# Optimization experiments

Measured on AMD Instinct MI355X. Metric: run time of the kernel, lower is better.

## Reference

```python
import jax, jax.numpy as jnp
import numpy as np


def setup_inputs() -> dict:
    key = jax.random.key(0)
    k1, k2, k3 = jax.random.split(key, 3)
    B, S, D_IN, V, D_OUT = 2, 2048, 1024, 32000, 4096
    x = jax.random.normal(k1, (B, S, D_IN), dtype=jnp.float32)
    W_ff = jax.random.normal(k2, (V, D_IN), dtype=jnp.float32) * (1.0 / np.sqrt(D_IN))
    b_ff = jnp.zeros((V,), dtype=jnp.float32)
    emb = jax.random.normal(k3, (V, D_OUT), dtype=jnp.float32)
    return {"x": x, "W_ff": W_ff, "b_ff": b_ff, "emb": emb}


def reference(x, W_ff, b_ff, emb):
    # logits: [B, S, V] = x @ W_ff^T + b
    logits = jnp.einsum('bsd,vd->bsv', x, W_ff) + b_ff
    probs = jax.nn.softmax(logits, axis=-1)  # [B, S, V]
    # soft embedding lookup: probs @ emb -> [B, S, D_OUT]
    out = jnp.einsum('bsv,vo->bso', probs, emb)
    return out
```

## Files before the change

### kernel.cpp

```cpp
#include <hip/hip_runtime.h>
#include <cstdint>

typedef unsigned short u16;
typedef __attribute__((ext_vector_type(8))) short short8;
typedef __attribute__((ext_vector_type(4))) short short4v;
typedef __attribute__((ext_vector_type(4))) float floatx4;

__device__ __forceinline__ u16 f2bf(float f) {
    unsigned u = __float_as_uint(f);
    return (u16)((u + 0x7FFFu + ((u >> 16) & 1u)) >> 16);
}
__device__ __forceinline__ float bf2f(u16 h) {
    return __uint_as_float(((unsigned)h) << 16);
}

__device__ __forceinline__ void gload16(u16* lds, const u16* g) {
    __builtin_amdgcn_global_load_lds(
        (const __attribute__((address_space(1))) unsigned*)g,
        (__attribute__((address_space(3))) unsigned*)lds,
        16, 0, 0);
}

#define CFENCE asm volatile("" ::: "memory")

__global__ void cast_kernel(const float* __restrict__ in, u16* __restrict__ out, int n4) {
    int stride = gridDim.x * blockDim.x;
    for (int i = blockIdx.x * blockDim.x + threadIdx.x; i < n4; i += stride) {
        float4 v = ((const float4*)in)[i];
        short4v o;
        o[0] = (short)f2bf(v.x);
        o[1] = (short)f2bf(v.y);
        o[2] = (short)f2bf(v.z);
        o[3] = (short)f2bf(v.w);
        ((short4v*)out)[i] = o;
    }
}

__global__ void transpose_cast(const float* __restrict__ E, u16* __restrict__ Et) {
    __shared__ u16 t[32][34];
    int bx = blockIdx.x, by = blockIdx.y;
    int x = threadIdx.x, y = threadIdx.y;
    long long c = (long long)bx * 32 + x;
    long long r0 = (long long)by * 32;
#pragma unroll
    for (int i = y; i < 32; i += 8)
        t[x][i] = f2bf(E[(r0 + i) * 4096 + c]);
    __syncthreads();
    int v = by * 32 + x;
#pragma unroll
    for (int i = y; i < 32; i += 8)
        Et[(long long)(bx * 32 + i) * 32000 + v] = t[i][x];
}

__global__ void rowsum_kernel(const u16* __restrict__ P, float* __restrict__ l, int V) {
    long long base = (long long)blockIdx.x * V;
    const short8* p8 = (const short8*)(P + base);
    int n8 = V >> 3;
    float s = 0.f;
    for (int c = threadIdx.x; c < n8; c += blockDim.x) {
        short8 v = p8[c];
#pragma unroll
        for (int j = 0; j < 8; ++j) s += bf2f((u16)v[j]);
    }
#pragma unroll
    for (int off = 32; off > 0; off >>= 1) s += __shfl_down(s, off, 64);
    __shared__ float red[4];
    if ((threadIdx.x & 63) == 0) red[threadIdx.x >> 6] = s;
    __syncthreads();
    if (threadIdx.x == 0) l[blockIdx.x] = red[0] + red[1] + red[2] + red[3];
}


__device__ __forceinline__ void stageA(u16* ldsh, const u16* Abase, int h, int t,
                                       int K, int w, int lane) {
#pragma unroll
    for (int i = 0; i < 2; ++i) {
        int r = w * 16 + i * 8 + (lane >> 3);
        int gc = (lane & 7) ^ ((r >> 1) & 7);
        int grow = ((r >> 6) << 7) + (h << 6) + (r & 63);
        gload16(ldsh + (w * 16 + i * 8) * 64,
                Abase + (long long)grow * K + t * 64 + gc * 8);
    }
}
__device__ __forceinline__ void stageB(u16* ldsh, const u16* Bbase, int h, int t,
                                       int K, int w, int lane) {
#pragma unroll
    for (int i = 0; i < 2; ++i) {
        int r = w * 16 + i * 8 + (lane >> 3);
        int gc = (lane & 7) ^ ((r >> 1) & 7);
        int grow = ((r >> 5) << 6) + (h << 5) + (r & 31);
        gload16(ldsh + (w * 16 + i * 8) * 64,
                Bbase + (long long)grow * K + t * 64 + gc * 8);
    }
}

template <int MH>
__device__ __forceinline__ void loadA(short8 af[4][2], const u16 (*lA)[128][64],
                                      int wm, int fRow, int fC) {
#pragma unroll
    for (int m = 0; m < 4; ++m)
#pragma unroll
        for (int kk = 0; kk < 2; ++kk) {
            int R = wm * 64 + m * 16 + fRow;
            int slot = (kk * 4 + fC) ^ ((R >> 1) & 7);
            af[m][kk] = *(const short8*)&lA[MH][R][slot * 8];
        }
}
template <int NH>
__device__ __forceinline__ void loadB(short8 bf[2][2], const u16 (*lB)[128][64],
                                      int wn, int fRow, int fC) {
#pragma unroll
    for (int n = 0; n < 2; ++n)
#pragma unroll
        for (int kk = 0; kk < 2; ++kk) {
            int R = wn * 32 + n * 16 + fRow;
            int slot = (kk * 4 + fC) ^ ((R >> 1) & 7);
            bf[n][kk] = *(const short8*)&lB[NH][R][slot * 8];
        }
}
template <int MH, int NH>
__device__ __forceinline__ void mfma16(floatx4 acc[8][4], short8 af[4][2],
                                       short8 bf[2][2]) {
#pragma unroll
    for (int m = 0; m < 4; ++m)
#pragma unroll
        for (int n = 0; n < 2; ++n)
#pragma unroll
            for (int kk = 0; kk < 2; ++kk)
                acc[MH * 4 + m][NH * 2 + n] = __builtin_amdgcn_mfma_f32_16x16x32_bf16(
                    af[m][kk], bf[n][kk], acc[MH * 4 + m][NH * 2 + n], 0, 0, 0);
}

template <int EP>
__global__ __launch_bounds__(512, 2)
void gemm8p(const u16* __restrict__ A, const u16* __restrict__ B,
            int M, int N, int K,
            const float* __restrict__ bias, u16* __restrict__ Pout,
            const float* __restrict__ rsum, float* __restrict__ Cout) {
    __shared__ u16 lds[2][2][2][128][64];
    const int tid = threadIdx.x;
    const int w = tid >> 6, lane = tid & 63;
    const int wm = w >> 2, wn = w & 3;
    const int fRow = lane & 15, fC = lane >> 4;

    int tm, tn;
    const int nTm = M >> 8;
    if (gridDim.x == 256) {
        const int x = blockIdx.x & 7, wgx = blockIdx.x >> 3;
        tm = (x & 3) * 4 + (wgx & 3);
        tn = (x >> 2) * 8 + (wgx >> 2);
    } else {
        const int q = gridDim.x >> 3;
        const int wg = (blockIdx.x & 7) * q + (blockIdx.x >> 3);
        tm = wg % nTm;
        tn = wg / nTm;
    }

    const u16* Abase = A + (long long)tm * 256 * K;
    const u16* Bbase = B + (long long)tn * 256 * K;
    const int NT = K >> 6;

    floatx4 acc[8][4] = {};
    short8 af[4][2], bf0[2][2], bf1[2][2];

    stageA(&lds[0][0][0][0][0], Abase, 0, 0, K, w, lane);
    stageB(&lds[0][1][0][0][0], Bbase, 0, 0, K, w, lane);
    stageB(&lds[0][1][1][0][0], Bbase, 1, 0, K, w, lane);
    stageA(&lds[0][0][1][0][0], Abase, 1, 0, K, w, lane);
    if (NT > 1) {
        stageA(&lds[1][0][0][0][0], Abase, 0, 1, K, w, lane);
        stageB(&lds[1][1][1][0][0], Bbase, 1, 1, K, w, lane);
        stageA(&lds[1][0][1][0][0], Abase, 1, 1, K, w, lane);
        asm volatile("s_waitcnt vmcnt(6)" ::: "memory");
    } else {
        asm volatile("s_waitcnt vmcnt(0)" ::: "memory");
    }
    __builtin_amdgcn_s_barrier();
    CFENCE;

    for (int t = 0; t < NT; ++t) {
        const int d = t & 1;
        const u16(*lA)[128][64] = lds[d][0];
        const u16(*lB)[128][64] = lds[d][1];

        loadA<0>(af, lA, wm, fRow, fC);
        loadB<0>(bf0, lB, wn, fRow, fC);
        loadB<1>(bf1, lB, wn, fRow, fC);
        if (t + 1 < NT) stageB(&lds[d ^ 1][1][0][0][0], Bbase, 0, t + 1, K, w, lane);
        asm volatile("s_waitcnt lgkmcnt(8)" ::: "memory");
        __builtin_amdgcn_s_barrier();
        asm volatile("s_waitcnt lgkmcnt(0)" ::: "memory");
        __builtin_amdgcn_s_setprio(1);
        mfma16<0, 0>(acc, af, bf0);
        __builtin_amdgcn_s_setprio(0);
        __builtin_amdgcn_s_barrier();
        CFENCE;

        if (t + 2 < NT) stageA(&lds[d][0][0][0][0], Abase, 0, t + 2, K, w, lane);
        __builtin_amdgcn_s_setprio(1);
        mfma16<0, 1>(acc, af, bf1);
        __builtin_amdgcn_s_setprio(0);
        CFENCE;

        loadA<1>(af, lA, wm, fRow, fC);
        if (t + 2 < NT) stageB(&lds[d][1][1][0][0], Bbase, 1, t + 2, K, w, lane);
        asm volatile("s_waitcnt lgkmcnt(4)" ::: "memory");
        __builtin_amdgcn_s_barrier();
        asm volatile("s_waitcnt lgkmcnt(0)" ::: "memory");
        __builtin_amdgcn_s_setprio(1);
        mfma16<1, 1>(acc, af, bf1);
        __builtin_amdgcn_s_setprio(0);
        __builtin_amdgcn_s_barrier();
        CFENCE;

        if (t + 2 < NT) {
            stageA(&lds[d][0][1][0][0], Abase, 1, t + 2, K, w, lane);
            asm volatile("s_waitcnt vmcnt(6)" ::: "memory");
        } else if (t + 1 < NT) {
            asm volatile("s_waitcnt vmcnt(0)" ::: "memory");
        }
        __builtin_amdgcn_s_barrier();
        __builtin_amdgcn_s_setprio(1);
        mfma16<1, 0>(acc, af, bf0);
        __builtin_amdgcn_s_setprio(0);
        __builtin_amdgcn_s_barrier();
        CFENCE;
    }

    const int rBase = tm * 256 + wm * 128;
    const int cBase = tn * 256 + wn * 64;
    const int rOff = (lane >> 4) * 4;
    const int cOff = lane & 15;
#pragma unroll
    for (int m = 0; m < 8; ++m) {
#pragma unroll
        for (int n = 0; n < 4; ++n) {
            const int col = cBase + n * 16 + cOff;
            if (EP == 0) {
                float bv = bias[col];
#pragma unroll
                for (int r = 0; r < 4; ++r) {
                    int row = rBase + m * 16 + rOff + r;
                    Pout[(long long)row * N + col] = f2bf(__expf(acc[m][n][r] + bv));
                }
            } else {
#pragma unroll
                for (int r = 0; r < 4; ++r) {
                    int row = rBase + m * 16 + rOff + r;
                    Cout[(long long)row * N + col] = acc[m][n][r] * (1.0f / rsum[row]);
                }
            }
        }
    }
}

extern "C" void kernel_launch(void* const* d_in, const int* in_sizes, int n_in,
                              void* d_out, int out_size, void* d_ws, size_t ws_size,
                              hipStream_t stream) {
    const float* x = (const float*)d_in[0];
    const float* W = (const float*)d_in[1];
    const float* b = (const float*)d_in[2];
    const float* E = (const float*)d_in[3];
    float* out = (float*)d_out;

    const int M = 4096, K1 = 1024, V = 32000, N2 = 4096;

    char* ws = (char*)d_ws;
    size_t off = 0;
    u16* xb = (u16*)(ws + off); off += (size_t)M * K1 * 2;
    u16* Wb = (u16*)(ws + off); off += (size_t)V * K1 * 2;
    u16* Et = (u16*)(ws + off); off += (size_t)N2 * V * 2;
    u16* P  = (u16*)(ws + off); off += (size_t)M * V * 2;
    float* l = (float*)(ws + off); off += (size_t)M * 4;

    cast_kernel<<<2048, 256, 0, stream>>>(x, xb, M * K1 / 4);
    cast_kernel<<<2048, 256, 0, stream>>>(W, Wb, V * K1 / 4);
    transpose_cast<<<dim3(N2 / 32, V / 32), dim3(32, 8), 0, stream>>>(E, Et);
    gemm8p<0><<<(M / 256) * (V / 256), 512, 0, stream>>>(xb, Wb, M, V, K1, b, P, nullptr, nullptr);
    rowsum_kernel<<<M, 256, 0, stream>>>(P, l, V);
    gemm8p<1><<<(M / 256) * (N2 / 256), 512, 0, stream>>>(P, Et, M, N2, V, nullptr, nullptr, l, out);
}
```

Before: 1.416 ms.

## Software-pipeline LDS fragment reads under MFMA blocks and cut barriers per K step

Restructures the GEMM main loop so the LDS reads of the A and B fragments for the next quadrant, including the next K tile, are issued interleaved with the current MFMA block. Two of the per-iteration barriers and the partial lgkmcnt waits are removed, and the stageA/stageB global prefetches are regrouped. The aim is to hide LDS read latency behind matrix work and cut synchronisation stalls. The risks are LDS read/write races from the reduced barriers and higher register pressure that could hurt the two-blocks-per-CU occupancy.

```diff
diff --git a/kernel.cpp b/kernel.cpp
--- a/kernel.cpp
+++ b/kernel.cpp
@@ -22,6 +22,7 @@
 }
 
 #define CFENCE asm volatile("" ::: "memory")
+#define MFMA_BF16 __builtin_amdgcn_mfma_f32_16x16x32_bf16
 
 __global__ void cast_kernel(const float* __restrict__ in, u16* __restrict__ out, int n4) {
     int stride = gridDim.x * blockDim.x;
@@ -94,41 +95,9 @@
     }
 }
 
-template <int MH>
-__device__ __forceinline__ void loadA(short8 af[4][2], const u16 (*lA)[128][64],
-                                      int wm, int fRow, int fC) {
-#pragma unroll
-    for (int m = 0; m < 4; ++m)
-#pragma unroll
-        for (int kk = 0; kk < 2; ++kk) {
-            int R = wm * 64 + m * 16 + fRow;
-            int slot = (kk * 4 + fC) ^ ((R >> 1) & 7);
-            af[m][kk] = *(const short8*)&lA[MH][R][slot * 8];
-        }
-}
-template <int NH>
-__device__ __forceinline__ void loadB(short8 bf[2][2], const u16 (*lB)[128][64],
-                                      int wn, int fRow, int fC) {
-#pragma unroll
-    for (int n = 0; n < 2; ++n)
-#pragma unroll
-        for (int kk = 0; kk < 2; ++kk) {
-            int R = wn * 32 + n * 16 + fRow;
-            int slot = (kk * 4 + fC) ^ ((R >> 1) & 7);
-            bf[n][kk] = *(const short8*)&lB[NH][R][slot * 8];
-        }
-}
-template <int MH, int NH>
-__device__ __forceinline__ void mfma16(floatx4 acc[8][4], short8 af[4][2],
-                                       short8 bf[2][2]) {
-#pragma unroll
-    for (int m = 0; m < 4; ++m)
-#pragma unroll
-        for (int n = 0; n < 2; ++n)
-#pragma unroll
-            for (int kk = 0; kk < 2; ++kk)
-                acc[MH * 4 + m][NH * 2 + n] = __builtin_amdgcn_mfma_f32_16x16x32_bf16(
-                    af[m][kk], bf[n][kk], acc[MH * 4 + m][NH * 2 + n], 0, 0, 0);
+__device__ __forceinline__ short8 ldsRead(const u16 (*lH)[64], int R, int kk, int fC) {
+    int slot = (kk * 4 + fC) ^ ((R >> 1) & 7);
+    return *(const short8*)&lH[R][slot * 8];
 }
 
 template <int EP>
@@ -177,53 +146,106 @@
     }
     __builtin_amdgcn_s_barrier();
     CFENCE;
+#pragma unroll
+    for (int m = 0; m < 4; ++m)
+#pragma unroll
+        for (int kk = 0; kk < 2; ++kk)
+            af[m][kk] = ldsRead(&lds[0][0][0][0], wm * 64 + m * 16 + fRow, kk, fC);
+#pragma unroll
+    for (int n = 0; n < 2; ++n)
+#pragma unroll
+        for (int kk = 0; kk < 2; ++kk)
+            bf1[n][kk] = ldsRead(&lds[0][1][1][0], wn * 32 + n * 16 + fRow, kk, fC);
 
     for (int t = 0; t < NT; ++t) {
         const int d = t & 1;
-        const u16(*lA)[128][64] = lds[d][0];
-        const u16(*lB)[128][64] = lds[d][1];
-
-        loadA<0>(af, lA, wm, fRow, fC);
-        loadB<0>(bf0, lB, wn, fRow, fC);
-        loadB<1>(bf1, lB, wn, fRow, fC);
+
+#pragma unroll
+        for (int n = 0; n < 2; ++n)
+#pragma unroll
+            for (int kk = 0; kk < 2; ++kk)
+                bf0[n][kk] = ldsRead(&lds[d][1][0][0], wn * 32 + n * 16 + fRow, kk, fC);
         if (t + 1 < NT) stageB(&lds[d ^ 1][1][0][0][0], Bbase, 0, t + 1, K, w, lane);
-        asm volatile("s_waitcnt lgkmcnt(8)" ::: "memory");
-        __builtin_amdgcn_s_barrier();
         asm volatile("s_waitcnt lgkmcnt(0)" ::: "memory");
+        __builtin_amdgcn_sched_barrier(0);
         __builtin_amdgcn_s_setprio(1);
-        mfma16<0, 0>(acc, af, bf0);
+#pragma unroll
+        for (int m = 0; m < 4; ++m)
+#pragma unroll
+            for (int n = 0; n < 2; ++n)
+#pragma unroll
+                for (int kk = 0; kk < 2; ++kk)
+                    acc[m][n] = MFMA_BF16(af[m][kk], bf0[n][kk], acc[m][n], 0, 0, 0);
         __builtin_amdgcn_s_setprio(0);
         __builtin_amdgcn_s_barrier();
         CFENCE;
 
-        if (t + 2 < NT) stageA(&lds[d][0][0][0][0], Abase, 0, t + 2, K, w, lane);
+        if (t + 2 < NT) {
+            stageA(&lds[d][0][0][0][0], Abase, 0, t + 2, K, w, lane);
+            stageB(&lds[d][1][1][0][0], Bbase, 1, t + 2, K, w, lane);
+        }
         __builtin_amdgcn_s_setprio(1);
-        mfma16<0, 1>(acc, af, bf1);
+#pragma unroll
+        for (int m = 0; m < 4; ++m) {
+#pragma unroll
+            for (int n = 0; n < 2; ++n)
+#pragma unroll
+                for (int kk = 0; kk < 2; ++kk)
+                    acc[m][2 + n] = MFMA_BF16(af[m][kk], bf1[n][kk], acc[m][2 + n], 0, 0, 0);
+#pragma unroll
+            for (int kk = 0; kk < 2; ++kk)
+                af[m][kk] = ldsRead(&lds[d][0][1][0], wm * 64 + m * 16 + fRow, kk, fC);
+        }
         __builtin_amdgcn_s_setprio(0);
-        CFENCE;
-
-        loadA<1>(af, lA, wm, fRow, fC);
-        if (t + 2 < NT) stageB(&lds[d][1][1][0][0], Bbase, 1, t + 2, K, w, lane);
-        asm volatile("s_waitcnt lgkmcnt(4)" ::: "memory");
-        __builtin_amdgcn_s_barrier();
-        asm volatile("s_waitcnt lgkmcnt(0)" ::: "memory");
+
         __builtin_amdgcn_s_setprio(1);
-        mfma16<1, 1>(acc, af, bf1);
+#pragma unroll
+        for (int m = 0; m < 4; ++m)
+#pragma unroll
+            for (int n = 0; n < 2; ++n)
+#pragma unroll
+                for (int kk = 0; kk < 2; ++kk)
+                    acc[4 + m][2 + n] = MFMA_BF16(af[m][kk], bf1[n][kk], acc[4 + m][2 + n], 0, 0, 0);
         __builtin_amdgcn_s_setprio(0);
+
+        if (t + 2 < NT) {
+            asm volatile("s_waitcnt vmcnt(4)" ::: "memory");
+        } else if (t + 1 < NT) {
+            asm volatile("s_waitcnt vmcnt(0)" ::: "memory");
+        }
         __builtin_amdgcn_s_barrier();
         CFENCE;
-
-        if (t + 2 < NT) {
-            stageA(&lds[d][0][1][0][0], Abase, 1, t + 2, K, w, lane);
-            asm volatile("s_waitcnt vmcnt(6)" ::: "memory");
-        } else if (t + 1 < NT) {
-            asm volatile("s_waitcnt vmcnt(0)" ::: "memory");
-        }
-        __builtin_amdgcn_s_barrier();
-        __builtin_amdgcn_s_setprio(1);
-        mfma16<1, 0>(acc, af, bf0);
-        __builtin_amdgcn_s_setprio(0);
-        __builtin_amdgcn_s_barrier();
+        if (t + 2 < NT) stageA(&lds[d][0][1][0][0], Abase, 1, t + 2, K, w, lane);
+        if (t + 1 < NT) {
+#pragma unroll
+            for (int n = 0; n < 2; ++n)
+#pragma unroll
+                for (int kk = 0; kk < 2; ++kk)
+                    bf1[n][kk] = ldsRead(&lds[d ^ 1][1][1][0], wn * 32 + n * 16 + fRow, kk, fC);
+            __builtin_amdgcn_s_setprio(1);
+#pragma unroll
+            for (int m = 0; m < 4; ++m) {
+#pragma unroll
+                for (int n = 0; n < 2; ++n)
+#pragma unroll
+                    for (int kk = 0; kk < 2; ++kk)
+                        acc[4 + m][n] = MFMA_BF16(af[m][kk], bf0[n][kk], acc[4 + m][n], 0, 0, 0);
+#pragma unroll
+                for (int kk = 0; kk < 2; ++kk)
+                    af[m][kk] = ldsRead(&lds[d ^ 1][0][0][0], wm * 64 + m * 16 + fRow, kk, fC);
+            }
+            __builtin_amdgcn_s_setprio(0);
+        } else {
+            __builtin_amdgcn_s_setprio(1);
+#pragma unroll
+            for (int m = 0; m < 4; ++m)
+#pragma unroll
+                for (int n = 0; n < 2; ++n)
+#pragma unroll
+                    for (int kk = 0; kk < 2; ++kk)
+                        acc[4 + m][n] = MFMA_BF16(af[m][kk], bf0[n][kk], acc[4 + m][n], 0, 0, 0);
+            __builtin_amdgcn_s_setprio(0);
+        }
         CFENCE;
     }
 
```

New measurement: 1.389 ms. About the same (-1.9%).
